# Performance work log

Hardware: AMD Instinct MI355X
Metric: run time of the kernel (lower is better)

## Reference

```python
import jax, jax.numpy as jnp
import numpy as np

N_NODES = 50000
IN_DIM = 128
HIDDEN = 64
OUT_DIM = 3
HEADS1 = 4
NEG_SLOPE = 0.2
EPS = 1e-16


def _glorot(key, shape):
    fan_in, fan_out = shape[0], shape[-1]
    lim = (6.0 / (fan_in + fan_out)) ** 0.5
    return jax.random.uniform(key, shape, jnp.float32, -lim, lim)


def setup_inputs() -> dict:
    key = jax.random.key(0)
    ks = jax.random.split(key, 12)
    x = jax.random.normal(ks[0], (N_NODES, IN_DIM), jnp.float32)
    edge_index = jax.random.randint(ks[1], (2, 400000), 0, N_NODES, jnp.int64)
    # layer 1: GATConv(in=128, out=64, heads=4)
    W1 = _glorot(ks[2], (IN_DIM, HEADS1 * HIDDEN))
    att_src1 = _glorot(ks[3], (HEADS1, HIDDEN))
    att_dst1 = _glorot(ks[4], (HEADS1, HIDDEN))
    b1 = jnp.zeros((HEADS1 * HIDDEN,), jnp.float32)
    # layer 2: GATConv(in=256, out=64, heads=1)
    W2 = _glorot(ks[5], (HEADS1 * HIDDEN, HIDDEN))
    att_src2 = _glorot(ks[6], (1, HIDDEN))
    att_dst2 = _glorot(ks[7], (1, HIDDEN))
    b2 = jnp.zeros((HIDDEN,), jnp.float32)
    # output linear
    Wout = _glorot(ks[8], (HIDDEN, OUT_DIM))
    bout = jnp.zeros((OUT_DIM,), jnp.float32)
    return {"x": x, "edge_index": edge_index, "W1": W1, "att_src1": att_src1,
            "att_dst1": att_dst1, "b1": b1, "W2": W2, "att_src2": att_src2,
            "att_dst2": att_dst2, "b2": b2, "Wout": Wout, "bout": bout}


def gat_conv(x, src, dst, W, a_src, a_dst, b, n_nodes):
    H, C = a_src.shape
    h = (x @ W).reshape(n_nodes, H, C)            # [N,H,C]
    a_s = jnp.sum(h * a_src[None], axis=-1)        # [N,H]
    a_d = jnp.sum(h * a_dst[None], axis=-1)        # [N,H]
    e = jax.nn.leaky_relu(a_s[src] + a_d[dst], NEG_SLOPE)  # [E,H]
    # segment softmax over incoming edges of each dst node
    m = jax.ops.segment_max(e, dst, num_segments=n_nodes)
    ex = jnp.exp(e - m[dst])
    denom = jax.ops.segment_sum(ex, dst, num_segments=n_nodes)
    alpha = ex / (denom[dst] + EPS)                # [E,H]
    msg = h[src] * alpha[..., None]                # [E,H,C]
    out = jax.ops.segment_sum(msg, dst, num_segments=n_nodes)
    return out.reshape(n_nodes, H * C) + b


def reference(x, edge_index, W1, att_src1, att_dst1, b1, W2, att_src2, att_dst2, b2, Wout, bout):
    n = x.shape[0]
    loop = jnp.arange(n, dtype=edge_index.dtype)
    src = jnp.concatenate([edge_index[0], loop])   # add self loops (PyG default)
    dst = jnp.concatenate([edge_index[1], loop])
    h = gat_conv(x, src, dst, W1, att_src1, att_dst1, b1, n)
    h = jax.nn.elu(h)
    h = gat_conv(h, src, dst, W2, att_src2, att_dst2, b2, n)
    h = jax.nn.elu(h)
    return h @ Wout + bout
```

## Files before the change

kernel.cpp:

```cpp
#include <hip/hip_runtime.h>
#include <hip/hip_bf16.h>
#include <math.h>

#define N_NODES  50000
#define IN_DIM   128
#define HIDDEN   64
#define OUT_DIM  3
#define HEADS1   4
#define E_RAW    400000
#define E_TOT    450000
#define NEG_SLOPE 0.2f
#define N_CHUNKS 49
#define WPREP_BLOCKS 128
#define EB_SC ((E_TOT + 255) / 256)
#define MB_GE (N_NODES / 16)

typedef __attribute__((ext_vector_type(8))) short bf16x8;
typedef __attribute__((ext_vector_type(4))) float f32x4;

static __device__ __forceinline__ float bfu(unsigned short u) {
    return __uint_as_float(((unsigned)u) << 16);
}
static __device__ __forceinline__ unsigned short f2b_bits(float v) {
    __hip_bfloat16 b = __float2bfloat16(v);
    return *reinterpret_cast<unsigned short*>(&b);
}

static __device__ __forceinline__ void get_edge(const int* __restrict__ ei, int is64,
                                                int e, int& s, int& d) {
    if (e >= E_RAW) { s = d = e - E_RAW; return; }
    if (is64) { s = ei[2 * e]; d = ei[2 * E_RAW + 2 * e]; }
    else      { s = ei[e];     d = ei[E_RAW + e]; }
    s = min(max(s, 0), N_NODES - 1);
    d = min(max(d, 0), N_NODES - 1);
}

static __device__ __forceinline__ int block_is64(const int* __restrict__ ei,
                                                 int e, bool valid, int* nzbuf) {
    bool real = valid && (e < E_RAW);
    int hv = real ? ei[2 * e + 1] : 0;
    if (threadIdx.x == 0) *nzbuf = 0;
    __syncthreads();
    if (__any(hv != 0) && (threadIdx.x & 63) == 0) *nzbuf = 1;
    __syncthreads();
    return (*nzbuf == 0);
}

__global__ void wprep_count_kernel(const float* __restrict__ W1, __hip_bfloat16* __restrict__ W1T,
                                   const float* __restrict__ W2, __hip_bfloat16* __restrict__ W2T,
                                   const int* __restrict__ ei, int* __restrict__ deg) {
    __shared__ int nz;
    int bid = blockIdx.x;
    if (bid < WPREP_BLOCKS) {
        int i = bid * 256 + threadIdx.x;
        if (i < 256 * 128) {
            int n = i >> 7, k = i & 127;
            *((unsigned short*)W1T + i) = f2b_bits(W1[k * 256 + n]);
        }
        if (i < 64 * 256) {
            int n = i >> 8, k = i & 255;
            *((unsigned short*)W2T + i) = f2b_bits(W2[k * 64 + n]);
        }
        return;
    }
    int e = (bid - WPREP_BLOCKS) * 256 + threadIdx.x;
    bool valid = e < E_TOT;
    int is64 = block_is64(ei, e, valid, &nz);
    if (!valid) return;
    int s, d;
    get_edge(ei, is64, e, s, d);
    atomicAdd(&deg[d], 1);
}

__global__ void scan_fused_kernel(const int* __restrict__ deg, int* __restrict__ row_ptr,
                                  int* __restrict__ cursor) {
    __shared__ int wsum[4];
    __shared__ int sbase;
    const int bid = blockIdx.x, t = threadIdx.x, wv = t >> 6, ln = t & 63;
    int base = 0;
    const int ng = bid * 256;
    for (int g = t; g < ng; g += 256) {
        int4 d = ((const int4*)deg)[g];
        base += (d.x + d.y) + (d.z + d.w);
    }
    #pragma unroll
    for (int off = 1; off < 64; off <<= 1) base += __shfl_xor(base, off, 64);
    if (ln == 0) wsum[wv] = base;
    __syncthreads();
    if (t == 0) sbase = wsum[0] + wsum[1] + wsum[2] + wsum[3];
    __syncthreads();
    base = sbase;
    int g = bid * 256 + t;
    int4 d = (g < 12500) ? ((const int4*)deg)[g] : make_int4(0, 0, 0, 0);
    int p0 = d.x, p1 = p0 + d.y, p2 = p1 + d.z, p3 = p2 + d.w;
    int s = p3;
    #pragma unroll
    for (int off = 1; off < 64; off <<= 1) {
        int u = __shfl_up(s, off, 64);
        if (ln >= off) s += u;
    }
    if (ln == 63) wsum[wv] = s;
    __syncthreads();
    int wbase = base;
    #pragma unroll
    for (int w = 0; w < 4; w++) wbase += (w < wv) ? wsum[w] : 0;
    int ex = wbase + s - p3;
    if (g < 12500) {
        int i = g * 4;
        row_ptr[i + 1] = ex + p0; row_ptr[i + 2] = ex + p1;
        row_ptr[i + 3] = ex + p2; row_ptr[i + 4] = ex + p3;
        cursor[i]     = ex;       cursor[i + 1]  = ex + p0;
        cursor[i + 2] = ex + p1;  cursor[i + 3]  = ex + p2;
    }
    if (bid == 0 && t == 0) row_ptr[0] = 0;
}

__global__ void __launch_bounds__(256) scatter_gemm_l1_kernel(
        const int* __restrict__ ei,
        int* __restrict__ cursor, int* __restrict__ csr_src,
        const float* __restrict__ x, const __hip_bfloat16* __restrict__ W1T,
        const float* __restrict__ att_s, const float* __restrict__ att_d,
        __hip_bfloat16* __restrict__ h1,
        float* __restrict__ asb4, float* __restrict__ adb4) {
    __shared__ unsigned short As[16][136];
    __shared__ __attribute__((aligned(16))) unsigned short hT[16][264];
    __shared__ int nz;
    if (blockIdx.x < EB_SC) {
        int e = blockIdx.x * 256 + threadIdx.x;
        bool valid = e < E_TOT;
        int is64 = block_is64(ei, e, valid, &nz);
        if (!valid) return;
        int s, d;
        get_edge(ei, is64, e, s, d);
        int pos = atomicAdd(&cursor[d], 1);
        csr_src[pos] = s;
        return;
    }
    const int tid = threadIdx.x;
    const int wave = tid >> 6, lane = tid & 63;
    const int quad = lane >> 4, m = lane & 15;
    const int row0 = (blockIdx.x - EB_SC) * 16;
    {
        int r = tid >> 4, seg = tid & 15;
        const float* xa = x + (size_t)(row0 + r) * IN_DIM + seg * 8;
        float4 u = *(const float4*)xa;
        float4 v = *(const float4*)(xa + 4);
        ushort4 p0, p1;
        p0.x = f2b_bits(u.x); p0.y = f2b_bits(u.y); p0.z = f2b_bits(u.z); p0.w = f2b_bits(u.w);
        p1.x = f2b_bits(v.x); p1.y = f2b_bits(v.y); p1.z = f2b_bits(v.z); p1.w = f2b_bits(v.w);
        *(ushort4*)&As[r][seg * 8]     = p0;
        *(ushort4*)&As[r][seg * 8 + 4] = p1;
    }
    __syncthreads();
    const int n0w = wave * 64;
    f32x4 acc0 = {0.f, 0.f, 0.f, 0.f}, acc1 = acc0, acc2 = acc0, acc3 = acc0;
    #pragma unroll
    for (int k0 = 0; k0 < IN_DIM; k0 += 32) {
        int kk = k0 + quad * 8;
        bf16x8 a = *(const bf16x8*)&As[m][kk];
        bf16x8 b0 = *(const bf16x8*)(W1T + (size_t)(n0w +  0 + m) * IN_DIM + kk);
        bf16x8 b1 = *(const bf16x8*)(W1T + (size_t)(n0w + 16 + m) * IN_DIM + kk);
        bf16x8 b2 = *(const bf16x8*)(W1T + (size_t)(n0w + 32 + m) * IN_DIM + kk);
        bf16x8 b3 = *(const bf16x8*)(W1T + (size_t)(n0w + 48 + m) * IN_DIM + kk);
        acc0 = __builtin_amdgcn_mfma_f32_16x16x32_bf16(a, b0, acc0, 0, 0, 0);
        acc1 = __builtin_amdgcn_mfma_f32_16x16x32_bf16(a, b1, acc1, 0, 0, 0);
        acc2 = __builtin_amdgcn_mfma_f32_16x16x32_bf16(a, b2, acc2, 0, 0, 0);
        acc3 = __builtin_amdgcn_mfma_f32_16x16x32_bf16(a, b3, acc3, 0, 0, 0);
    }
    float ats0 = att_s[n0w +  0 + m], atd0 = att_d[n0w +  0 + m];
    float ats1 = att_s[n0w + 16 + m], atd1 = att_d[n0w + 16 + m];
    float ats2 = att_s[n0w + 32 + m], atd2 = att_d[n0w + 32 + m];
    float ats3 = att_s[n0w + 48 + m], atd3 = att_d[n0w + 48 + m];
    #pragma unroll
    for (int i = 0; i < 4; i++) {
        int r = quad * 4 + i;
        hT[r][n0w +  0 + m] = f2b_bits(acc0[i]);
        hT[r][n0w + 16 + m] = f2b_bits(acc1[i]);
        hT[r][n0w + 32 + m] = f2b_bits(acc2[i]);
        hT[r][n0w + 48 + m] = f2b_bits(acc3[i]);
        float ps = acc0[i] * ats0 + acc1[i] * ats1 + acc2[i] * ats2 + acc3[i] * ats3;
        float pd = acc0[i] * atd0 + acc1[i] * atd1 + acc2[i] * atd2 + acc3[i] * atd3;
        #pragma unroll
        for (int off = 1; off < 16; off <<= 1) {
            ps += __shfl_xor(ps, off, 16);
            pd += __shfl_xor(pd, off, 16);
        }
        if (m == 0) {
            asb4[(row0 + r) * 4 + wave] = ps;
            adb4[(row0 + r) * 4 + wave] = pd;
        }
    }
    __syncthreads();
    {
        unsigned short* hrow = (unsigned short*)h1;
        int r0 = tid >> 5, c0 = tid & 31;
        *(bf16x8*)(hrow + (size_t)(row0 + r0) * 256 + c0 * 8) = *(const bf16x8*)&hT[r0][c0 * 8];
        int S = tid + 256;
        int r1 = S >> 5, c1 = S & 31;
        *(bf16x8*)(hrow + (size_t)(row0 + r1) * 256 + c1 * 8) = *(const bf16x8*)&hT[r1][c1 * 8];
    }
}

__global__ void __launch_bounds__(1024, 8) gat_gather4_l2_kernel(
        const int* __restrict__ row_ptr, const int* __restrict__ csr_src,
        const float* __restrict__ asb4, const float* __restrict__ adb4,
        const __hip_bfloat16* __restrict__ h1, const float* __restrict__ bias,
        const __hip_bfloat16* __restrict__ W2T,
        const float* __restrict__ att_s, const float* __restrict__ att_d,
        __hip_bfloat16* __restrict__ h2,
        float* __restrict__ asb, float* __restrict__ adb) {
    __shared__ __attribute__((aligned(16))) unsigned short As[16][264];
    __shared__ __attribute__((aligned(16))) unsigned short hT2[16][72];
    __shared__ float sPS[4][16];
    __shared__ float sPD[4][16];
    const int tid = threadIdx.x;
    const int wave = tid >> 6, lane = tid & 63;
    const int row0 = blockIdx.x * 16;
    const int c    = lane & 31;
    const int slot = lane >> 5;
    const int head = c >> 3;
    const int eidx0 = lane >> 2;
    const int hh   = lane & 3;

    {
        const int n = row0 + wave;
        int b = row_ptr[n], e = row_ptr[n + 1];
        float adnh = adb4[n * 4 + hh];
        float acc[8];
        #pragma unroll
        for (int i = 0; i < 8; i++) acc[i] = 0.f;
        float l = 0.f;
        for (int c0 = b; c0 < e; c0 += 16) {
            int cnt = min(16, e - c0);
            int s_all = (lane < cnt) ? csr_src[c0 + lane] : 0;
            int sE = __shfl(s_all, eidx0, 64);
            float w_all = 0.f;
            if (eidx0 < cnt) {
                float v = asb4[sE * 4 + hh] + adnh;
                v = (v > 0.f) ? v : NEG_SLOPE * v;
                w_all = __expf(v);
            }
            #pragma unroll 2
            for (int k = 0; k < cnt; k += 2) {
                int eidx = k + slot;
                int s = __shfl(s_all, eidx, 64);
                float w = __shfl(w_all, eidx * 4 + head, 64);
                bf16x8 f = *(const bf16x8*)(h1 + (size_t)s * 256 + c * 8);
                l += w;
                #pragma unroll
                for (int i = 0; i < 8; i++)
                    acc[i] += w * bfu((unsigned short)f[i]);
            }
        }
        #pragma unroll
        for (int i = 0; i < 8; i++) acc[i] += __shfl_xor(acc[i], 32, 64);
        l += __shfl_xor(l, 32, 64);
        if (lane < 32) {
            float il = 1.f / (l + 1e-16f);
            float4 b0 = *(const float4*)(bias + c * 8);
            float4 b1 = *(const float4*)(bias + c * 8 + 4);
            float r[8];
            r[0] = acc[0] * il + b0.x; r[1] = acc[1] * il + b0.y;
            r[2] = acc[2] * il + b0.z; r[3] = acc[3] * il + b0.w;
            r[4] = acc[4] * il + b1.x; r[5] = acc[5] * il + b1.y;
            r[6] = acc[6] * il + b1.z; r[7] = acc[7] * il + b1.w;
            bf16x8 st;
            #pragma unroll
            for (int i = 0; i < 8; i++) {
                float v = (r[i] > 0.f) ? r[i] : expm1f(r[i]);
                st[i] = (short)f2b_bits(v);
            }
            *(bf16x8*)&As[wave][c * 8] = st;
        }
    }
    __syncthreads();

    if (wave < 4) {
        const int quad = lane >> 4, m = lane & 15;
        const int n0 = wave * 16;
        f32x4 acc = {0.f, 0.f, 0.f, 0.f};
        #pragma unroll
        for (int k0 = 0; k0 < 256; k0 += 32) {
            int kk = k0 + quad * 8;
            bf16x8 a = *(const bf16x8*)&As[m][kk];
            bf16x8 bfr = *(const bf16x8*)(W2T + (size_t)(n0 + m) * 256 + kk);
            acc = __builtin_amdgcn_mfma_f32_16x16x32_bf16(a, bfr, acc, 0, 0, 0);
        }
        float ats = att_s[n0 + m], atd = att_d[n0 + m];
        #pragma unroll
        for (int i = 0; i < 4; i++) {
            int r = quad * 4 + i;
            hT2[r][n0 + m] = f2b_bits(acc[i]);
            float ps = acc[i] * ats;
            float pd = acc[i] * atd;
            #pragma unroll
            for (int off = 1; off < 16; off <<= 1) {
                ps += __shfl_xor(ps, off, 16);
                pd += __shfl_xor(pd, off, 16);
            }
            if (m == 0) {
                sPS[wave][r] = ps;
                sPD[wave][r] = pd;
            }
        }
    }
    __syncthreads();
    if (tid < 128) {
        int r = tid >> 3, cs = tid & 7;
        *(bf16x8*)((unsigned short*)h2 + (size_t)(row0 + r) * 64 + cs * 8) =
            *(const bf16x8*)&hT2[r][cs * 8];
    }
    if (tid < 16) {
        float ps = sPS[0][tid] + sPS[1][tid] + sPS[2][tid] + sPS[3][tid];
        float pd = sPD[0][tid] + sPD[1][tid] + sPD[2][tid] + sPD[3][tid];
        asb[row0 + tid] = ps;
        adb[row0 + tid] = pd;
    }
}

__global__ void __launch_bounds__(256) gat_gather1_out_kernel(
        const int* __restrict__ row_ptr, const int* __restrict__ csr_src,
        const float* __restrict__ asb, const float* __restrict__ adb,
        const __hip_bfloat16* __restrict__ h2, const float* __restrict__ bias,
        const float* __restrict__ Wout, const float* __restrict__ bout,
        float* __restrict__ out) {
    int wave = threadIdx.x >> 6;
    int lane = threadIdx.x & 63;
    int n = blockIdx.x * 4 + wave;
    if (n >= N_NODES) return;
    int b = row_ptr[n], e = row_ptr[n + 1];
    const int c    = lane & 7;
    const int slot = lane >> 3;
    float adn = adb[n];
    float acc[8];
    #pragma unroll
    for (int i = 0; i < 8; i++) acc[i] = 0.f;
    float l = 0.f;
    for (int c0 = b; c0 < e; c0 += 64) {
        int cnt = min(64, e - c0);
        int s_all = (lane < cnt) ? csr_src[c0 + lane] : 0;
        float w_all = 0.f;
        if (lane < cnt) {
            float v = asb[s_all] + adn;
            v = (v > 0.f) ? v : NEG_SLOPE * v;
            w_all = __expf(v);
        }
        #pragma unroll 2
        for (int k = 0; k < cnt; k += 8) {
            int eidx = k + slot;
            int s = __shfl(s_all, eidx, 64);
            float w = __shfl(w_all, eidx, 64);
            bf16x8 f = *(const bf16x8*)(h2 + (size_t)s * 64 + c * 8);
            l += w;
            #pragma unroll
            for (int i = 0; i < 8; i++)
                acc[i] += w * bfu((unsigned short)f[i]);
        }
    }
    #pragma unroll
    for (int off = 8; off < 64; off <<= 1) {
        #pragma unroll
        for (int i = 0; i < 8; i++) acc[i] += __shfl_xor(acc[i], off, 64);
        l += __shfl_xor(l, off, 64);
    }
    float il = 1.f / (l + 1e-16f);
    float4 b0 = *(const float4*)(bias + c * 8);
    float4 b1 = *(const float4*)(bias + c * 8 + 4);
    float v[8];
    v[0] = acc[0] * il + b0.x; v[1] = acc[1] * il + b0.y;
    v[2] = acc[2] * il + b0.z; v[3] = acc[3] * il + b0.w;
    v[4] = acc[4] * il + b1.x; v[5] = acc[5] * il + b1.y;
    v[6] = acc[6] * il + b1.z; v[7] = acc[7] * il + b1.w;
    #pragma unroll
    for (int i = 0; i < 8; i++) v[i] = (v[i] > 0.f) ? v[i] : expm1f(v[i]);
    const float* wp = Wout + c * 24;
    float o0 = 0.f, o1 = 0.f, o2 = 0.f;
    #pragma unroll
    for (int i = 0; i < 8; i++) {
        o0 += v[i] * wp[i * 3 + 0];
        o1 += v[i] * wp[i * 3 + 1];
        o2 += v[i] * wp[i * 3 + 2];
    }
    #pragma unroll
    for (int off = 1; off < 8; off <<= 1) {
        o0 += __shfl_xor(o0, off, 64);
        o1 += __shfl_xor(o1, off, 64);
        o2 += __shfl_xor(o2, off, 64);
    }
    if (lane == 0) {
        out[n * OUT_DIM + 0] = o0 + bout[0];
        out[n * OUT_DIM + 1] = o1 + bout[1];
        out[n * OUT_DIM + 2] = o2 + bout[2];
    }
}

extern "C" void kernel_launch(void* const* d_in, const int* in_sizes, int n_in,
                              void* d_out, int out_size, void* d_ws, size_t ws_size,
                              hipStream_t stream) {
    const float* x    = (const float*)d_in[0];
    const int*   ei   = (const int*)d_in[1];
    const float* W1   = (const float*)d_in[2];
    const float* as1  = (const float*)d_in[3];
    const float* ad1  = (const float*)d_in[4];
    const float* b1   = (const float*)d_in[5];
    const float* W2   = (const float*)d_in[6];
    const float* as2  = (const float*)d_in[7];
    const float* ad2  = (const float*)d_in[8];
    const float* b2v  = (const float*)d_in[9];
    const float* Wout = (const float*)d_in[10];
    const float* bout = (const float*)d_in[11];
    float* out = (float*)d_out;

    float* ws    = (float*)d_ws;
    float* asb4  = ws + 16;
    float* adb4  = asb4 + (size_t)N_NODES * 4;
    float* asb1  = adb4 + (size_t)N_NODES * 4;
    float* adb1  = asb1 + N_NODES;
    __hip_bfloat16* h1     = (__hip_bfloat16*)(adb1 + N_NODES);
    __hip_bfloat16* h2     = (__hip_bfloat16*)(h1 + (size_t)N_NODES * 256);
    __hip_bfloat16* W1T    = (__hip_bfloat16*)(h2 + (size_t)N_NODES * 64);
    __hip_bfloat16* W2T    = W1T + 256 * 128;
    int* deg     = (int*)(W2T + 64 * 256);
    int* row_ptr = deg + N_NODES;
    int* cursor  = row_ptr + N_NODES + 16;
    int* csr_src = cursor + N_NODES;

    const int EB = EB_SC;
    const int AB = (N_NODES + 3) / 4;

    hipMemsetAsync(deg, 0, (size_t)N_NODES * sizeof(int), stream);
    wprep_count_kernel<<<WPREP_BLOCKS + EB, 256, 0, stream>>>(W1, W1T, W2, W2T, ei, deg);
    scan_fused_kernel<<<N_CHUNKS, 256, 0, stream>>>(deg, row_ptr, cursor);

    scatter_gemm_l1_kernel<<<EB + MB_GE, 256, 0, stream>>>(ei, cursor, csr_src,
                                                           x, W1T, as1, ad1, h1, asb4, adb4);

    gat_gather4_l2_kernel<<<MB_GE, 1024, 0, stream>>>(row_ptr, csr_src, asb4, adb4, h1, b1,
                                                      W2T, as2, ad2, h2, asb1, adb1);

    gat_gather1_out_kernel<<<AB, 256, 0, stream>>>(row_ptr, csr_src, asb1, adb1, h2,
                                                   b2v, Wout, bout, out);
}
```

Baseline: 260.9 us.

## Replace block-tiled layer-2 GEMM with per-wave shuffle-fed MFMA projection

Restructures the layer-1 aggregation plus layer-2 projection kernel so each 64-lane wave handles one node end to end. The aggregated row is broadcast through shuffles into MFMA operands instead of staged in shared memory. This removes shared memory and the two block-wide barriers and uses 256-thread blocks. The cost is that every node reloads the full W2 weight matrix and runs 16x redundant MFMA rows, since only one output row is used.

```diff
diff --git a/kernel.cpp b/kernel.cpp
--- a/kernel.cpp
+++ b/kernel.cpp
@@ -201,7 +201,7 @@
     }
 }
 
-__global__ void __launch_bounds__(1024, 8) gat_gather4_l2_kernel(
+__global__ void __launch_bounds__(256) gat_gather4_gemv_kernel(
         const int* __restrict__ row_ptr, const int* __restrict__ csr_src,
         const float* __restrict__ asb4, const float* __restrict__ adb4,
         const __hip_bfloat16* __restrict__ h1, const float* __restrict__ bias,
@@ -209,112 +209,99 @@
         const float* __restrict__ att_s, const float* __restrict__ att_d,
         __hip_bfloat16* __restrict__ h2,
         float* __restrict__ asb, float* __restrict__ adb) {
-    __shared__ __attribute__((aligned(16))) unsigned short As[16][264];
-    __shared__ __attribute__((aligned(16))) unsigned short hT2[16][72];
-    __shared__ float sPS[4][16];
-    __shared__ float sPD[4][16];
-    const int tid = threadIdx.x;
-    const int wave = tid >> 6, lane = tid & 63;
-    const int row0 = blockIdx.x * 16;
+    const int wave = threadIdx.x >> 6;
+    const int lane = threadIdx.x & 63;
+    const int n = blockIdx.x * 4 + wave;
+    int b = row_ptr[n], e = row_ptr[n + 1];
     const int c    = lane & 31;
     const int slot = lane >> 5;
     const int head = c >> 3;
     const int eidx0 = lane >> 2;
     const int hh   = lane & 3;
-
-    {
-        const int n = row0 + wave;
-        int b = row_ptr[n], e = row_ptr[n + 1];
-        float adnh = adb4[n * 4 + hh];
-        float acc[8];
-        #pragma unroll
-        for (int i = 0; i < 8; i++) acc[i] = 0.f;
-        float l = 0.f;
-        for (int c0 = b; c0 < e; c0 += 16) {
-            int cnt = min(16, e - c0);
-            int s_all = (lane < cnt) ? csr_src[c0 + lane] : 0;
-            int sE = __shfl(s_all, eidx0, 64);
-            float w_all = 0.f;
-            if (eidx0 < cnt) {
-                float v = asb4[sE * 4 + hh] + adnh;
-                v = (v > 0.f) ? v : NEG_SLOPE * v;
-                w_all = __expf(v);
-            }
-            #pragma unroll 2
-            for (int k = 0; k < cnt; k += 2) {
-                int eidx = k + slot;
-                int s = __shfl(s_all, eidx, 64);
-                float w = __shfl(w_all, eidx * 4 + head, 64);
-                bf16x8 f = *(const bf16x8*)(h1 + (size_t)s * 256 + c * 8);
-                l += w;
-                #pragma unroll
-                for (int i = 0; i < 8; i++)
-                    acc[i] += w * bfu((unsigned short)f[i]);
-            }
-        }
-        #pragma unroll
-        for (int i = 0; i < 8; i++) acc[i] += __shfl_xor(acc[i], 32, 64);
-        l += __shfl_xor(l, 32, 64);
-        if (lane < 32) {
-            float il = 1.f / (l + 1e-16f);
-            float4 b0 = *(const float4*)(bias + c * 8);
-            float4 b1 = *(const float4*)(bias + c * 8 + 4);
-            float r[8];
-            r[0] = acc[0] * il + b0.x; r[1] = acc[1] * il + b0.y;
-            r[2] = acc[2] * il + b0.z; r[3] = acc[3] * il + b0.w;
-            r[4] = acc[4] * il + b1.x; r[5] = acc[5] * il + b1.y;
-            r[6] = acc[6] * il + b1.z; r[7] = acc[7] * il + b1.w;
-            bf16x8 st;
+    float adnh = adb4[n * 4 + hh];
+    float acc[8];
+    #pragma unroll
+    for (int i = 0; i < 8; i++) acc[i] = 0.f;
+    float l = 0.f;
+    for (int c0 = b; c0 < e; c0 += 16) {
+        int cnt = min(16, e - c0);
+        int s_all = (lane < cnt) ? csr_src[c0 + lane] : 0;
+        int sE = __shfl(s_all, eidx0, 64);
+        float w_all = 0.f;
+        if (eidx0 < cnt) {
+            float v = asb4[sE * 4 + hh] + adnh;
+            v = (v > 0.f) ? v : NEG_SLOPE * v;
+            w_all = __expf(v);
+        }
+        #pragma unroll 2
+        for (int k = 0; k < cnt; k += 2) {
+            int eidx = k + slot;
+            int s = __shfl(s_all, eidx, 64);
+            float w = __shfl(w_all, eidx * 4 + head, 64);
+            bf16x8 f = *(const bf16x8*)(h1 + (size_t)s * 256 + c * 8);
+            l += w;
             #pragma unroll
-            for (int i = 0; i < 8; i++) {
-                float v = (r[i] > 0.f) ? r[i] : expm1f(r[i]);
-                st[i] = (short)f2b_bits(v);
-            }
-            *(bf16x8*)&As[wave][c * 8] = st;
-        }
-    }
-    __syncthreads();
-
-    if (wave < 4) {
-        const int quad = lane >> 4, m = lane & 15;
-        const int n0 = wave * 16;
-        f32x4 acc = {0.f, 0.f, 0.f, 0.f};
+            for (int i = 0; i < 8; i++)
+                acc[i] += w * bfu((unsigned short)f[i]);
+        }
+    }
+    #pragma unroll
+    for (int i = 0; i < 8; i++) acc[i] += __shfl_xor(acc[i], 32, 64);
+    l += __shfl_xor(l, 32, 64);
+    float il = 1.f / (l + 1e-16f);
+    float4 b0 = *(const float4*)(bias + c * 8);
+    float4 b1 = *(const float4*)(bias + c * 8 + 4);
+    float r[8];
+    r[0] = acc[0] * il + b0.x; r[1] = acc[1] * il + b0.y;
+    r[2] = acc[2] * il + b0.z; r[3] = acc[3] * il + b0.w;
+    r[4] = acc[4] * il + b1.x; r[5] = acc[5] * il + b1.y;
+    r[6] = acc[6] * il + b1.z; r[7] = acc[7] * il + b1.w;
+    bf16x8 st;
+    #pragma unroll
+    for (int i = 0; i < 8; i++) {
+        float v = (r[i] > 0.f) ? r[i] : expm1f(r[i]);
+        st[i] = (short)f2b_bits(v);
+    }
+    const int m = lane & 15, quad = lane >> 4;
+    const int* sp = (const int*)&st;
+    float ps = 0.f, pd = 0.f;
+    unsigned short* hp = (unsigned short*)h2 + (size_t)n * 64;
+    #pragma unroll
+    for (int pass = 0; pass < 2; pass++) {
+        const int g0 = pass * 32;
+        f32x4 o0 = {0.f, 0.f, 0.f, 0.f}, o1 = o0;
         #pragma unroll
         for (int k0 = 0; k0 < 256; k0 += 32) {
+            int src = (k0 >> 3) + quad;
+            bf16x8 a;
+            int* ap = (int*)&a;
+            ap[0] = __shfl(sp[0], src, 64);
+            ap[1] = __shfl(sp[1], src, 64);
+            ap[2] = __shfl(sp[2], src, 64);
+            ap[3] = __shfl(sp[3], src, 64);
             int kk = k0 + quad * 8;
-            bf16x8 a = *(const bf16x8*)&As[m][kk];
-            bf16x8 bfr = *(const bf16x8*)(W2T + (size_t)(n0 + m) * 256 + kk);
-            acc = __builtin_amdgcn_mfma_f32_16x16x32_bf16(a, bfr, acc, 0, 0, 0);
-        }
-        float ats = att_s[n0 + m], atd = att_d[n0 + m];
+            bf16x8 w0 = *(const bf16x8*)(W2T + (size_t)(g0 +  0 + m) * 256 + kk);
+            bf16x8 w1 = *(const bf16x8*)(W2T + (size_t)(g0 + 16 + m) * 256 + kk);
+            o0 = __builtin_amdgcn_mfma_f32_16x16x32_bf16(a, w0, o0, 0, 0, 0);
+            o1 = __builtin_amdgcn_mfma_f32_16x16x32_bf16(a, w1, o1, 0, 0, 0);
+        }
+        if (quad == 0) {
+            hp[g0 +  0 + m] = f2b_bits(o0[0]);
+            hp[g0 + 16 + m] = f2b_bits(o1[0]);
+            ps += o0[0] * att_s[g0 + m] + o1[0] * att_s[g0 + 16 + m];
+            pd += o0[0] * att_d[g0 + m] + o1[0] * att_d[g0 + 16 + m];
+        }
+    }
+    if (quad == 0) {
         #pragma unroll
-        for (int i = 0; i < 4; i++) {
-            int r = quad * 4 + i;
-            hT2[r][n0 + m] = f2b_bits(acc[i]);
-            float ps = acc[i] * ats;
-            float pd = acc[i] * atd;
-            #pragma unroll
-            for (int off = 1; off < 16; off <<= 1) {
-                ps += __shfl_xor(ps, off, 16);
-                pd += __shfl_xor(pd, off, 16);
-            }
-            if (m == 0) {
-                sPS[wave][r] = ps;
-                sPD[wave][r] = pd;
-            }
-        }
-    }
-    __syncthreads();
-    if (tid < 128) {
-        int r = tid >> 3, cs = tid & 7;
-        *(bf16x8*)((unsigned short*)h2 + (size_t)(row0 + r) * 64 + cs * 8) =
-            *(const bf16x8*)&hT2[r][cs * 8];
-    }
-    if (tid < 16) {
-        float ps = sPS[0][tid] + sPS[1][tid] + sPS[2][tid] + sPS[3][tid];
-        float pd = sPD[0][tid] + sPD[1][tid] + sPD[2][tid] + sPD[3][tid];
-        asb[row0 + tid] = ps;
-        adb[row0 + tid] = pd;
+        for (int off = 1; off < 16; off <<= 1) {
+            ps += __shfl_xor(ps, off, 16);
+            pd += __shfl_xor(pd, off, 16);
+        }
+        if (m == 0) {
+            asb[n] = ps;
+            adb[n] = pd;
+        }
     }
 }
 
@@ -435,8 +422,8 @@
     scatter_gemm_l1_kernel<<<EB + MB_GE, 256, 0, stream>>>(ei, cursor, csr_src,
                                                            x, W1T, as1, ad1, h1, asb4, adb4);
 
-    gat_gather4_l2_kernel<<<MB_GE, 1024, 0, stream>>>(row_ptr, csr_src, asb4, adb4, h1, b1,
-                                                      W2T, as2, ad2, h2, asb1, adb1);
+    gat_gather4_gemv_kernel<<<AB, 256, 0, stream>>>(row_ptr, csr_src, asb4, adb4, h1, b1,
+                                                    W2T, as2, ad2, h2, asb1, adb1);
 
     gat_gather1_out_kernel<<<AB, 256, 0, stream>>>(row_ptr, csr_src, asb1, adb1, h2,
                                                    b2v, Wout, bout, out);
```

After: 405.3 us. 55.4% more time.
